# Kernel tuning notes

Hardware: AMD Instinct MI355X
Metric: run time of the kernel (lower is better)

Reference implementation:

```python
import jax, jax.numpy as jnp
import numpy as np

B, CI, CO, H, W = 32, 64, 64, 128, 128
M1, M2 = 32, 32


def setup_inputs() -> dict:
    key = jax.random.key(0)
    kx, k1r, k1i, k2r, k2i = jax.random.split(key, 5)
    scale = 1.0 / (CI * CO)
    x = jax.random.normal(kx, (B, CI, H, W), dtype=jnp.float32)
    mk = lambda k: jax.random.uniform(k, (CI, CO, M1, M2), dtype=jnp.float32,
                                      minval=-scale, maxval=scale)
    return {"x": x, "w1r": mk(k1r), "w1i": mk(k1i), "w2r": mk(k2r), "w2i": mk(k2i)}


def reference(x, w1r, w1i, w2r, w2i):
    # x: [B, CI, H, W] real. Full 2D FFT over the last two dims.
    x_ft = jnp.fft.fft2(x.astype(jnp.complex64))  # [B, CI, H, W]
    w1 = jax.lax.complex(w1r, w1i)  # [CI, CO, M1, M2]
    w2 = jax.lax.complex(w2r, w2i)
    # Truncated-mode complex channel mixing with conjugated weights.
    top = jnp.einsum('bixy,ioxy->boxy', x_ft[:, :, :M1, :M2], jnp.conj(w1))
    bot = jnp.einsum('bixy,ioxy->boxy', x_ft[:, :, -M1:, :M2], jnp.conj(w2))
    # Scatter into rfft-width spectral tensor (as in the original code).
    Wout = W // 2 + 1
    out_ft = jnp.zeros((B, CO, H, Wout), dtype=jnp.complex64)
    out_ft = out_ft.at[:, :, :M1, :M2].set(top)
    out_ft = out_ft.at[:, :, -M1:, :M2].set(bot)
    # Full inverse 2D FFT, take real part. Output: [B, CO, H, Wout].
    return jnp.real(jnp.fft.ifft2(out_ft))
```

## Files before the change

### kernel.cpp

```cpp
#include <hip/hip_runtime.h>
#include <math.h>

#define PI2 6.28318530717958647692f


typedef short bf16x8 __attribute__((ext_vector_type(8)));
typedef float f32x4 __attribute__((ext_vector_type(4)));

static __device__ __forceinline__ ushort f2bf(float f) {
    uint u = __float_as_uint(f);
    u += 0x7FFFu + ((u >> 16) & 1u);
    return (ushort)(u >> 16);
}
static __device__ __forceinline__ float bf2f(ushort h) {
    return __uint_as_float(((uint)h) << 16);
}

__global__ void k_einit(ushort* __restrict__ e1, ushort* __restrict__ e2,
                        ushort* __restrict__ ec, ushort* __restrict__ ew) {
    int id = blockIdx.x * 256 + threadIdx.x;
    if (id < 8192) {
        int w = id & 127, col = id >> 7;
        int ky = col & 31, csel = col >> 5;
        int m = (ky * w) & 127;
        float sv, cv;
        sincosf((float)m * (PI2 / 128.0f), &sv, &cv);
        float val = csel ? -sv : cv;
        ushort hi = f2bf(val);
        int ui = col * 128 + (w ^ ((col & 7) << 3));
        e1[ui] = hi;
        e1[8192 + ui] = f2bf(val - bf2f(hi));
    } else if (id < 16384) {
        int id2 = id - 8192;
        int h = id2 & 127, kxi = id2 >> 7;
        int kx = (kxi < 32) ? kxi : (kxi + 64);
        int m = (kx * h) & 127;
        float sv, cv;
        sincosf((float)m * (PI2 / 128.0f), &sv, &cv);
        float er = cv, ei = -sv;
        int ui = kxi * 128 + (h ^ ((kxi & 7) << 3));
        ushort eh = f2bf(er);
        e2[ui] = eh;
        e2[8192 + ui] = f2bf(er - bf2f(eh));
        ushort ih = f2bf(ei);
        e2[16384 + ui] = ih;
        e2[24576 + ui] = f2bf(ei - bf2f(ih));
    } else if (id < 32768) {
        int id2 = id - 16384;
        int j = id2 & 7, ln = (id2 >> 3) & 15, kq = (id2 >> 7) & 3,
            kk = (id2 >> 9) & 3, mt = id2 >> 11;
        int h = mt * 16 + ln;
        int k = kk * 32 + kq * 8 + j;
        int kc = (k < 64) ? k : (k - 64);
        int kx = (kc < 32) ? kc : (kc + 64);
        int m = (kx * h) & 127;
        float sv, cv;
        sincosf((float)m * (PI2 / 128.0f), &sv, &cv);
        float val = ((k < 64) ? cv : sv) * (1.0f / 8320.0f);
        ushort hi = f2bf(val);
        ec[id2] = hi;
        ec[16384 + id2] = f2bf(val - bf2f(hi));
    } else if (id < 40448) {
        int id3 = id - 32768;
        int off = id3 % 2560, pe = id3 / 2560;
        int j = off & 7, ln = (off >> 3) & 15, kq = (off >> 7) & 3, nt1 = off >> 9;
        int ky = kq * 8 + j, w = nt1 * 16 + ln;
        float val = 0.0f;
        if (w < 65) {
            int m = (w * ky) % 65;
            float sv, cv;
            sincosf((float)m * (PI2 / 65.0f), &sv, &cv);
            val = (pe == 0) ? cv : ((pe == 1) ? sv : -sv);
        }
        ushort hi = f2bf(val);
        ew[pe * 5120 + off] = hi;
        ew[pe * 5120 + 2560 + off] = f2bf(val - bf2f(hi));
    }
}

__global__ __launch_bounds__(256) void k_f1(const float* __restrict__ x,
                                            const ushort* __restrict__ eimg,
                                            ushort* __restrict__ yimg) {
    __shared__ ushort lds[32768];
    const int bi = blockIdx.x;
    const int hbase = blockIdx.y * 64;
    const int t = threadIdx.x;

    {
        const uint4* esrc = (const uint4*)eimg;
        uint4* edst = (uint4*)lds;
        for (int i = t; i < 2048; i += 256) edst[i] = esrc[i];
    }

    const float* xp = x + (size_t)bi * 16384 + (size_t)hbase * 128;
    for (int i = 0; i < 4; i++) {
        int idx = i * 2048 + t * 8;
        int row = idx >> 7, w0 = idx & 127;
        float4 v0 = *(const float4*)&xp[idx];
        float4 v1 = *(const float4*)&xp[idx + 4];
        float vv[8] = {v0.x, v0.y, v0.z, v0.w, v1.x, v1.y, v1.z, v1.w};
        ushort h[8], l[8];
#pragma unroll
        for (int j = 0; j < 8; j++) {
            h[j] = f2bf(vv[j]);
            l[j] = f2bf(vv[j] - bf2f(h[j]));
        }
        uint4 hp, lp;
        hp.x = (uint)h[0] | ((uint)h[1] << 16);
        hp.y = (uint)h[2] | ((uint)h[3] << 16);
        hp.z = (uint)h[4] | ((uint)h[5] << 16);
        hp.w = (uint)h[6] | ((uint)h[7] << 16);
        lp.x = (uint)l[0] | ((uint)l[1] << 16);
        lp.y = (uint)l[2] | ((uint)l[3] << 16);
        lp.z = (uint)l[4] | ((uint)l[5] << 16);
        lp.w = (uint)l[6] | ((uint)l[7] << 16);
        int ui = row * 128 + (w0 ^ ((row & 7) << 3));
        *(uint4*)&lds[16384 + ui] = hp;
        *(uint4*)&lds[24576 + ui] = lp;
    }
    __syncthreads();

    const int lane = t & 63, wid = t >> 6;
    const int ln = lane & 15, kq = lane >> 4;
    f32x4 acc[4] = {};
#pragma unroll
    for (int kk = 0; kk < 4; kk++) {
        int k0 = kk * 32 + kq * 8;
        int arow = wid * 16 + ln;
        int aui = arow * 128 + (k0 ^ ((arow & 7) << 3));
        bf16x8 ah = *(bf16x8*)&lds[16384 + aui];
        bf16x8 al = *(bf16x8*)&lds[24576 + aui];
#pragma unroll
        for (int nt = 0; nt < 4; nt++) {
            int col = nt * 16 + ln;
            int bui = col * 128 + (k0 ^ ((col & 7) << 3));
            bf16x8 bh = *(bf16x8*)&lds[bui];
            bf16x8 bl = *(bf16x8*)&lds[8192 + bui];
            acc[nt] = __builtin_amdgcn_mfma_f32_16x16x32_bf16(ah, bh, acc[nt], 0, 0, 0);
            acc[nt] = __builtin_amdgcn_mfma_f32_16x16x32_bf16(ah, bl, acc[nt], 0, 0, 0);
            acc[nt] = __builtin_amdgcn_mfma_f32_16x16x32_bf16(al, bh, acc[nt], 0, 0, 0);
        }
    }

    ushort* yp = yimg + (size_t)bi * 16384;
    const int h0 = hbase + wid * 16 + kq * 4;
#pragma unroll
    for (int nt = 0; nt < 4; nt++) {
        int col = nt * 16 + ln;
        int ky = col & 31, c = col >> 5;
        ushort4 h4, l4;
        float v0 = acc[nt][0], v1 = acc[nt][1], v2 = acc[nt][2], v3 = acc[nt][3];
        h4.x = f2bf(v0); l4.x = f2bf(v0 - bf2f(h4.x));
        h4.y = f2bf(v1); l4.y = f2bf(v1 - bf2f(h4.y));
        h4.z = f2bf(v2); l4.z = f2bf(v2 - bf2f(h4.z));
        h4.w = f2bf(v3); l4.w = f2bf(v3 - bf2f(h4.w));
        int hs = h0 ^ ((ky & 7) << 3);
        *(ushort4*)&yp[(c * 2) * 4096 + ky * 128 + hs] = h4;
        *(ushort4*)&yp[(c * 2 + 1) * 4096 + ky * 128 + hs] = l4;
    }
}

__global__ __launch_bounds__(512) void k_f2(const ushort* __restrict__ yimg,
                                            const ushort* __restrict__ e2img,
                                            float2* __restrict__ xf) {
    __shared__ ushort lds[32768];
    const int t = threadIdx.x;
    const int bi0 = blockIdx.x * 8;

    uint4 R[4];
    {
        const uint4* ys = (const uint4*)(yimg + (size_t)bi0 * 16384);
#pragma unroll
        for (int c = 0; c < 4; c++) R[c] = ys[c * 512 + t];
    }
    {
        const uint4* es = (const uint4*)e2img;
        uint4* ed = (uint4*)lds;
        for (int i = t; i < 4096; i += 512) ed[i] = es[i];
    }
    __syncthreads();
    const int lane = t & 63, wid = t >> 6;
    const int ln = lane & 15, kq = lane >> 4;
    const int mt = wid >> 1, nt = wid & 1;
    const int arow = mt * 16 + ln;
    const int bcol = nt * 16 + ln;
    bf16x8 Erh[4], Erl[4], Eih[4], Eil[4];
#pragma unroll
    for (int kk = 0; kk < 4; kk++) {
        int k0 = kk * 32 + kq * 8;
        int ao = arow * 128 + (k0 ^ ((arow & 7) << 3));
        Erh[kk] = *(const bf16x8*)&lds[ao];
        Erl[kk] = *(const bf16x8*)&lds[8192 + ao];
        Eih[kk] = *(const bf16x8*)&lds[16384 + ao];
        Eil[kk] = *(const bf16x8*)&lds[24576 + ao];
    }
    __syncthreads();
    {
        uint4* yd = (uint4*)lds;
#pragma unroll
        for (int c = 0; c < 4; c++) yd[c * 512 + t] = R[c];
    }
    __syncthreads();

    int cur = 0;
    for (int j = 0; j < 8; j++) {
        const int bi = bi0 + j;
        if (j < 7) {
            const uint4* ys = (const uint4*)(yimg + (size_t)(bi + 1) * 16384);
#pragma unroll
            for (int c = 0; c < 4; c++) R[c] = ys[c * 512 + t];
        }
        const ushort* yb = &lds[cur * 16384];
        f32x4 P1 = {}, P2 = {}, P3 = {}, P4 = {};
#pragma unroll
        for (int kk = 0; kk < 4; kk++) {
            int k0 = kk * 32 + kq * 8;
            int bo = bcol * 128 + (k0 ^ ((bcol & 7) << 3));
            bf16x8 Yrh = *(const bf16x8*)&yb[bo];
            bf16x8 Yrl = *(const bf16x8*)&yb[4096 + bo];
            bf16x8 Yih = *(const bf16x8*)&yb[8192 + bo];
            bf16x8 Yil = *(const bf16x8*)&yb[12288 + bo];
            P1 = __builtin_amdgcn_mfma_f32_16x16x32_bf16(Erh[kk], Yrh, P1, 0, 0, 0);
            P1 = __builtin_amdgcn_mfma_f32_16x16x32_bf16(Erh[kk], Yrl, P1, 0, 0, 0);
            P1 = __builtin_amdgcn_mfma_f32_16x16x32_bf16(Erl[kk], Yrh, P1, 0, 0, 0);
            P2 = __builtin_amdgcn_mfma_f32_16x16x32_bf16(Eih[kk], Yih, P2, 0, 0, 0);
            P2 = __builtin_amdgcn_mfma_f32_16x16x32_bf16(Eih[kk], Yil, P2, 0, 0, 0);
            P2 = __builtin_amdgcn_mfma_f32_16x16x32_bf16(Eil[kk], Yih, P2, 0, 0, 0);
            P3 = __builtin_amdgcn_mfma_f32_16x16x32_bf16(Erh[kk], Yih, P3, 0, 0, 0);
            P3 = __builtin_amdgcn_mfma_f32_16x16x32_bf16(Erh[kk], Yil, P3, 0, 0, 0);
            P3 = __builtin_amdgcn_mfma_f32_16x16x32_bf16(Erl[kk], Yih, P3, 0, 0, 0);
            P4 = __builtin_amdgcn_mfma_f32_16x16x32_bf16(Eih[kk], Yrh, P4, 0, 0, 0);
            P4 = __builtin_amdgcn_mfma_f32_16x16x32_bf16(Eih[kk], Yrl, P4, 0, 0, 0);
            P4 = __builtin_amdgcn_mfma_f32_16x16x32_bf16(Eil[kk], Yrh, P4, 0, 0, 0);
        }
        float2* xp = xf + (size_t)bi * 2048 + (size_t)(mt * 16 + kq * 4) * 32 + bcol;
#pragma unroll
        for (int r = 0; r < 4; r++)
            xp[(size_t)r * 32] = make_float2(P1[r] - P2[r], P3[r] + P4[r]);
        if (j < 7) {
            uint4* yd = (uint4*)&lds[(cur ^ 1) * 16384];
#pragma unroll
            for (int c = 0; c < 4; c++) yd[c * 512 + t] = R[c];
            __syncthreads();
            cur ^= 1;
        }
    }
}

__global__ __launch_bounds__(512) void k_mix(const float2* __restrict__ xf,
                                             const float* __restrict__ w1r, const float* __restrict__ w1i,
                                             const float* __restrict__ w2r, const float* __restrict__ w2i,
                                             float2* __restrict__ tt) {
    __shared__ float2 xfs[8192];
    const int kxi = blockIdx.x;
    const int b0 = blockIdx.y * 8;
    const int t = threadIdx.x;
    const int ky = t & 31, grp = t >> 5;
    const int o0 = grp * 4;
    const float* wr = (kxi < 32) ? w1r : w2r;
    const float* wi = (kxi < 32) ? w1i : w2i;
    const int kxim = kxi & 31;
    float accr[8][4], acci[8][4];
    for (int jb = 0; jb < 8; jb++)
        for (int jo = 0; jo < 4; jo++) { accr[jb][jo] = 0.0f; acci[jb][jo] = 0.0f; }

    for (int stage = 0; stage < 2; stage++) {
        const int ibase = stage * 32;
        __syncthreads();
        for (int idx = t; idx < 8192; idx += 512) {
            int b = idx >> 10, ii = (idx >> 5) & 31, kk = idx & 31;
            size_t g = ((size_t)(b0 + b) * 64 + (ibase + ii)) * 2048 + (size_t)kxi * 32 + kk;
            xfs[idx] = xf[g];
        }
        __syncthreads();
        for (int ii = 0; ii < 32; ii++) {
            const int i = ibase + ii;
            float wr4[4], wi4[4];
#pragma unroll
            for (int jo = 0; jo < 4; jo++) {
                size_t g = ((size_t)i * 64 + (o0 + jo)) * 1024 + (size_t)kxim * 32 + ky;
                wr4[jo] = wr[g]; wi4[jo] = wi[g];
            }
#pragma unroll
            for (int jb = 0; jb < 8; jb++) {
                float2 xv = xfs[(jb << 10) + (ii << 5) + ky];
#pragma unroll
                for (int jo = 0; jo < 4; jo++) {
                    accr[jb][jo] += xv.x * wr4[jo] + xv.y * wi4[jo];
                    acci[jb][jo] += xv.y * wr4[jo] - xv.x * wi4[jo];
                }
            }
        }
    }
    for (int jb = 0; jb < 8; jb++)
        for (int jo = 0; jo < 4; jo++) {
            size_t g = ((size_t)(b0 + jb) * 64 + (o0 + jo)) * 2048 + (size_t)kxi * 32 + ky;
            tt[g] = make_float2(accr[jb][jo], acci[jb][jo]);
        }
}

#define G1_TILE(TT, ZRv, ZIv)                                                  \
    do {                                                                       \
        int mt1_ = (TT) & 3, nt1_ = (TT) >> 2;                                 \
        int arow_ = mt1_ * 16 + ln;                                            \
        int aad_ = arow_ * 40 + ((kq ^ (arow_ & 3)) << 3);                     \
        bf16x8 TRh_ = *(const bf16x8*)&lds[aad_];                              \
        bf16x8 TRl_ = *(const bf16x8*)&lds[2560 + aad_];                       \
        bf16x8 TIh_ = *(const bf16x8*)&lds[5120 + aad_];                       \
        bf16x8 TIl_ = *(const bf16x8*)&lds[7680 + aad_];                       \
        const ushort* bp_ = ew + (((nt1_ * 4 + kq) * 16 + ln) * 8);            \
        bf16x8 CWh_ = *(const bf16x8*)(bp_);                                   \
        bf16x8 CWl_ = *(const bf16x8*)(bp_ + 2560);                            \
        bf16x8 SWh_ = *(const bf16x8*)(bp_ + 5120);                            \
        bf16x8 SWl_ = *(const bf16x8*)(bp_ + 7680);                            \
        bf16x8 SNh_ = *(const bf16x8*)(bp_ + 10240);                           \
        bf16x8 SNl_ = *(const bf16x8*)(bp_ + 12800);                           \
        ZRv = __builtin_amdgcn_mfma_f32_16x16x32_bf16(TRh_, CWh_, ZRv, 0, 0, 0); \
        ZRv = __builtin_amdgcn_mfma_f32_16x16x32_bf16(TRh_, CWl_, ZRv, 0, 0, 0); \
        ZRv = __builtin_amdgcn_mfma_f32_16x16x32_bf16(TRl_, CWh_, ZRv, 0, 0, 0); \
        ZRv = __builtin_amdgcn_mfma_f32_16x16x32_bf16(TIh_, SNh_, ZRv, 0, 0, 0); \
        ZRv = __builtin_amdgcn_mfma_f32_16x16x32_bf16(TIh_, SNl_, ZRv, 0, 0, 0); \
        ZRv = __builtin_amdgcn_mfma_f32_16x16x32_bf16(TIl_, SNh_, ZRv, 0, 0, 0); \
        ZIv = __builtin_amdgcn_mfma_f32_16x16x32_bf16(TRh_, SWh_, ZIv, 0, 0, 0); \
        ZIv = __builtin_amdgcn_mfma_f32_16x16x32_bf16(TRh_, SWl_, ZIv, 0, 0, 0); \
        ZIv = __builtin_amdgcn_mfma_f32_16x16x32_bf16(TRl_, SWh_, ZIv, 0, 0, 0); \
        ZIv = __builtin_amdgcn_mfma_f32_16x16x32_bf16(TIh_, CWh_, ZIv, 0, 0, 0); \
        ZIv = __builtin_amdgcn_mfma_f32_16x16x32_bf16(TIh_, CWl_, ZIv, 0, 0, 0); \
        ZIv = __builtin_amdgcn_mfma_f32_16x16x32_bf16(TIl_, CWh_, ZIv, 0, 0, 0); \
    } while (0)

#define Z_STORE(TT, ZRv, ZIv)                                                  \
    do {                                                                       \
        int mt1_ = (TT) & 3, nt1_ = (TT) >> 2;                                 \
        int w_ = nt1_ * 16 + ln;                                               \
        int kxi_ = mt1_ * 16 + kq * 4;                                         \
        int octr_ = kxi_ >> 3, sub_ = kxi_ & 7;                                \
        int adr_ = w_ * 128 + ((octr_ ^ (w_ & 7)) << 3) + sub_;                \
        int adi_ = w_ * 128 + (((octr_ + 8) ^ (w_ & 7)) << 3) + sub_;          \
        ushort4 rh_, rl_, ih_, il_;                                            \
        float v0_ = ZRv[0], v1_ = ZRv[1], v2_ = ZRv[2], v3_ = ZRv[3];          \
        rh_.x = f2bf(v0_); rl_.x = f2bf(v0_ - bf2f(rh_.x));                    \
        rh_.y = f2bf(v1_); rl_.y = f2bf(v1_ - bf2f(rh_.y));                    \
        rh_.z = f2bf(v2_); rl_.z = f2bf(v2_ - bf2f(rh_.z));                    \
        rh_.w = f2bf(v3_); rl_.w = f2bf(v3_ - bf2f(rh_.w));                    \
        v0_ = -ZIv[0]; v1_ = -ZIv[1]; v2_ = -ZIv[2]; v3_ = -ZIv[3];            \
        ih_.x = f2bf(v0_); il_.x = f2bf(v0_ - bf2f(ih_.x));                    \
        ih_.y = f2bf(v1_); il_.y = f2bf(v1_ - bf2f(ih_.y));                    \
        ih_.z = f2bf(v2_); il_.z = f2bf(v2_ - bf2f(ih_.z));                    \
        ih_.w = f2bf(v3_); il_.w = f2bf(v3_ - bf2f(ih_.w));                    \
        *(ushort4*)&lds[adr_] = rh_;                                           \
        *(ushort4*)&lds[10240 + adr_] = rl_;                                   \
        *(ushort4*)&lds[adi_] = ih_;                                           \
        *(ushort4*)&lds[10240 + adi_] = il_;                                   \
    } while (0)

__global__ __launch_bounds__(512) void k_inv(const float2* __restrict__ tt,
                                             const ushort* __restrict__ ec,
                                             const ushort* __restrict__ ew,
                                             float* __restrict__ out) {
    __shared__ ushort lds[20480];
    const int bo = blockIdx.x, t = threadIdx.x;
    const int lane = t & 63, wid = t >> 6;
    const int ln = lane & 15, kq = lane >> 4;

    bf16x8 ECh[4], ECl[4];
#pragma unroll
    for (int kk = 0; kk < 4; kk++) {
        const ushort* p = ec + ((((wid * 4 + kk) * 4 + kq) * 16 + ln) * 8);
        ECh[kk] = *(const bf16x8*)p;
        ECl[kk] = *(const bf16x8*)(p + 16384);
    }

    const float2* tp = tt + (size_t)bo * 2048;
    for (int i = t; i < 2048; i += 512) {
        float2 v = tp[i];
        int row = i >> 5, ky = i & 31;
        int ad = row * 40 + ((((ky >> 3) ^ (row & 3))) << 3) + (ky & 7);
        ushort rh = f2bf(v.x), ih = f2bf(v.y);
        lds[ad] = rh;
        lds[2560 + ad] = f2bf(v.x - bf2f(rh));
        lds[5120 + ad] = ih;
        lds[7680 + ad] = f2bf(v.y - bf2f(ih));
    }
    __syncthreads();

    f32x4 ZR0 = {}, ZI0 = {}, ZR1 = {}, ZI1 = {}, ZR2 = {}, ZI2 = {};
    G1_TILE(wid, ZR0, ZI0);
    G1_TILE(wid + 8, ZR1, ZI1);
    if (wid < 4) G1_TILE(wid + 16, ZR2, ZI2);
    __syncthreads();

    Z_STORE(wid, ZR0, ZI0);
    Z_STORE(wid + 8, ZR1, ZI1);
    if (wid < 4) Z_STORE(wid + 16, ZR2, ZI2);
    __syncthreads();

    f32x4 acc[5] = {};
#pragma unroll
    for (int nt = 0; nt < 5; nt++) {
        int w = nt * 16 + ln;
#pragma unroll
        for (int kk = 0; kk < 4; kk++) {
            int oct = kk * 4 + kq;
            int ad = w * 128 + ((oct ^ (w & 7)) << 3);
            bf16x8 Bh = *(const bf16x8*)&lds[ad];
            bf16x8 Bl = *(const bf16x8*)&lds[10240 + ad];
            acc[nt] = __builtin_amdgcn_mfma_f32_16x16x32_bf16(ECh[kk], Bh, acc[nt], 0, 0, 0);
            acc[nt] = __builtin_amdgcn_mfma_f32_16x16x32_bf16(ECh[kk], Bl, acc[nt], 0, 0, 0);
            acc[nt] = __builtin_amdgcn_mfma_f32_16x16x32_bf16(ECl[kk], Bh, acc[nt], 0, 0, 0);
        }
    }
    float* op = out + (size_t)bo * 8320;
    const int h0 = wid * 16 + kq * 4;
#pragma unroll
    for (int nt = 0; nt < 5; nt++) {
        int w = nt * 16 + ln;
        if (w < 65) {
#pragma unroll
            for (int r = 0; r < 4; r++)
                op[(h0 + r) * 65 + w] = acc[nt][r];
        }
    }
}

extern "C" void kernel_launch(void* const* d_in, const int* in_sizes, int n_in,
                              void* d_out, int out_size, void* d_ws, size_t ws_size,
                              hipStream_t stream) {
    const float* x   = (const float*)d_in[0];
    const float* w1r = (const float*)d_in[1];
    const float* w1i = (const float*)d_in[2];
    const float* w2r = (const float*)d_in[3];
    const float* w2i = (const float*)d_in[4];
    float2* ws = (float2*)d_ws;

    ushort* yimg = (ushort*)ws;
    float2* ta   = ws;
    float2* xfa  = ws + 8388608;
    ushort* e1img = (ushort*)(ws + 12582912);
    ushort* e2img = (ushort*)(ws + 12587008);
    ushort* ecimg = (ushort*)(ws + 12595200);
    ushort* ewimg = (ushort*)(ws + 12603392);
    float* out = (float*)d_out;

    k_einit<<<160, 256, 0, stream>>>(e1img, e2img, ecimg, ewimg);
    k_f1<<<dim3(2048, 2), 256, 0, stream>>>(x, e1img, yimg);
    k_f2<<<256, 512, 0, stream>>>(yimg, e2img, xfa);
    k_mix<<<dim3(64, 4), 512, 0, stream>>>(xfa, w1r, w1i, w2r, w2i, ta);
    k_inv<<<2048, 512, 0, stream>>>(ta, ecimg, ewimg, out);
}
```

Before: 401.2 us.

## Rewrite spectral channel mixing as split-bf16 MFMA GEMMs with mode-major layout

```diff
diff --git a/kernel.cpp b/kernel.cpp
--- a/kernel.cpp
+++ b/kernel.cpp
@@ -233,10 +233,10 @@
             P4 = __builtin_amdgcn_mfma_f32_16x16x32_bf16(Eih[kk], Yrl, P4, 0, 0, 0);
             P4 = __builtin_amdgcn_mfma_f32_16x16x32_bf16(Eil[kk], Yrh, P4, 0, 0, 0);
         }
-        float2* xp = xf + (size_t)bi * 2048 + (size_t)(mt * 16 + kq * 4) * 32 + bcol;
+        float2* xp = xf + (size_t)(mt * 16 + kq * 4) * 65536 + (size_t)bi * 32 + bcol;
 #pragma unroll
         for (int r = 0; r < 4; r++)
-            xp[(size_t)r * 32] = make_float2(P1[r] - P2[r], P3[r] + P4[r]);
+            xp[(size_t)r * 65536] = make_float2(P1[r] - P2[r], P3[r] + P4[r]);
         if (j < 7) {
             uint4* yd = (uint4*)&lds[(cur ^ 1) * 16384];
 #pragma unroll
@@ -247,56 +247,93 @@
     }
 }
 
-__global__ __launch_bounds__(512) void k_mix(const float2* __restrict__ xf,
+__global__ __launch_bounds__(256) void k_mix(const float2* __restrict__ xf,
                                              const float* __restrict__ w1r, const float* __restrict__ w1i,
                                              const float* __restrict__ w2r, const float* __restrict__ w2i,
                                              float2* __restrict__ tt) {
-    __shared__ float2 xfs[8192];
+    __shared__ ushort lds[24576];
     const int kxi = blockIdx.x;
-    const int b0 = blockIdx.y * 8;
+    const int ky  = blockIdx.y;
     const int t = threadIdx.x;
-    const int ky = t & 31, grp = t >> 5;
-    const int o0 = grp * 4;
     const float* wr = (kxi < 32) ? w1r : w2r;
     const float* wi = (kxi < 32) ? w1i : w2i;
     const int kxim = kxi & 31;
-    float accr[8][4], acci[8][4];
-    for (int jb = 0; jb < 8; jb++)
-        for (int jo = 0; jo < 4; jo++) { accr[jb][jo] = 0.0f; acci[jb][jo] = 0.0f; }
-
-    for (int stage = 0; stage < 2; stage++) {
-        const int ibase = stage * 32;
-        __syncthreads();
-        for (int idx = t; idx < 8192; idx += 512) {
-            int b = idx >> 10, ii = (idx >> 5) & 31, kk = idx & 31;
-            size_t g = ((size_t)(b0 + b) * 64 + (ibase + ii)) * 2048 + (size_t)kxi * 32 + kk;
-            xfs[idx] = xf[g];
-        }
-        __syncthreads();
-        for (int ii = 0; ii < 32; ii++) {
-            const int i = ibase + ii;
-            float wr4[4], wi4[4];
-#pragma unroll
-            for (int jo = 0; jo < 4; jo++) {
-                size_t g = ((size_t)i * 64 + (o0 + jo)) * 1024 + (size_t)kxim * 32 + ky;
-                wr4[jo] = wr[g]; wi4[jo] = wi[g];
-            }
-#pragma unroll
-            for (int jb = 0; jb < 8; jb++) {
-                float2 xv = xfs[(jb << 10) + (ii << 5) + ky];
-#pragma unroll
-                for (int jo = 0; jo < 4; jo++) {
-                    accr[jb][jo] += xv.x * wr4[jo] + xv.y * wi4[jo];
-                    acci[jb][jo] += xv.y * wr4[jo] - xv.x * wi4[jo];
-                }
-            }
-        }
-    }
-    for (int jb = 0; jb < 8; jb++)
-        for (int jo = 0; jo < 4; jo++) {
-            size_t g = ((size_t)(b0 + jb) * 64 + (o0 + jo)) * 2048 + (size_t)kxi * 32 + ky;
-            tt[g] = make_float2(accr[jb][jo], acci[jb][jo]);
-        }
+
+    const float2* xp = xf + (size_t)kxi * 65536 + ky;
+#pragma unroll
+    for (int k = 0; k < 8; k++) {
+        int idx = t + 256 * k;
+        float2 v = xp[(size_t)idx * 32];
+        int b = idx >> 6, i = idx & 63;
+        int ad = b * 64 + ((((i >> 3) ^ (b & 7))) << 3) + (i & 7);
+        ushort rh = f2bf(v.x), ih = f2bf(v.y);
+        lds[ad] = rh;
+        lds[2048 + ad] = f2bf(v.x - bf2f(rh));
+        lds[4096 + ad] = ih;
+        lds[6144 + ad] = f2bf(v.y - bf2f(ih));
+    }
+    const size_t wbase = (size_t)kxim * 32 + ky;
+#pragma unroll
+    for (int k = 0; k < 16; k++) {
+        int p = t + 256 * k;
+        int o = p >> 6, i = p & 63;
+        size_t g = ((size_t)i * 64 + o) * 1024 + wbase;
+        float wrv = wr[g], wiv = wi[g];
+        int ad = 8192 + o * 64 + ((((i >> 3) ^ (o & 7))) << 3) + (i & 7);
+        ushort rh = f2bf(wrv), ih = f2bf(wiv);
+        lds[ad] = rh;
+        lds[4096 + ad] = f2bf(wrv - bf2f(rh));
+        lds[8192 + ad] = ih;
+        lds[12288 + ad] = f2bf(wiv - bf2f(ih));
+    }
+    __syncthreads();
+
+    const int lane = t & 63, wid = t >> 6;
+    const int ln = lane & 15, kq = lane >> 4;
+    const int mt = wid & 1;
+    f32x4 Tr[2] = {}, TiA[2] = {}, TiB[2] = {};
+#pragma unroll
+    for (int u = 0; u < 2; u++) {
+        int nt = (wid >> 1) + u * 2;
+        int o = nt * 16 + ln;
+        int b = mt * 16 + ln;
+#pragma unroll
+        for (int kk = 0; kk < 2; kk++) {
+            int aad = b * 64 + (((kk * 4 + kq) ^ (b & 7)) << 3);
+            bf16x8 Xrh = *(const bf16x8*)&lds[aad];
+            bf16x8 Xrl = *(const bf16x8*)&lds[2048 + aad];
+            bf16x8 Xih = *(const bf16x8*)&lds[4096 + aad];
+            bf16x8 Xil = *(const bf16x8*)&lds[6144 + aad];
+            int bad = 8192 + o * 64 + (((kk * 4 + kq) ^ (o & 7)) << 3);
+            bf16x8 Wrh = *(const bf16x8*)&lds[bad];
+            bf16x8 Wrl = *(const bf16x8*)&lds[4096 + bad];
+            bf16x8 Wih = *(const bf16x8*)&lds[8192 + bad];
+            bf16x8 Wil = *(const bf16x8*)&lds[12288 + bad];
+            Tr[u] = __builtin_amdgcn_mfma_f32_16x16x32_bf16(Xrh, Wrh, Tr[u], 0, 0, 0);
+            Tr[u] = __builtin_amdgcn_mfma_f32_16x16x32_bf16(Xrh, Wrl, Tr[u], 0, 0, 0);
+            Tr[u] = __builtin_amdgcn_mfma_f32_16x16x32_bf16(Xrl, Wrh, Tr[u], 0, 0, 0);
+            Tr[u] = __builtin_amdgcn_mfma_f32_16x16x32_bf16(Xih, Wih, Tr[u], 0, 0, 0);
+            Tr[u] = __builtin_amdgcn_mfma_f32_16x16x32_bf16(Xih, Wil, Tr[u], 0, 0, 0);
+            Tr[u] = __builtin_amdgcn_mfma_f32_16x16x32_bf16(Xil, Wih, Tr[u], 0, 0, 0);
+            TiA[u] = __builtin_amdgcn_mfma_f32_16x16x32_bf16(Xih, Wrh, TiA[u], 0, 0, 0);
+            TiA[u] = __builtin_amdgcn_mfma_f32_16x16x32_bf16(Xih, Wrl, TiA[u], 0, 0, 0);
+            TiA[u] = __builtin_amdgcn_mfma_f32_16x16x32_bf16(Xil, Wrh, TiA[u], 0, 0, 0);
+            TiB[u] = __builtin_amdgcn_mfma_f32_16x16x32_bf16(Xrh, Wih, TiB[u], 0, 0, 0);
+            TiB[u] = __builtin_amdgcn_mfma_f32_16x16x32_bf16(Xrh, Wil, TiB[u], 0, 0, 0);
+            TiB[u] = __builtin_amdgcn_mfma_f32_16x16x32_bf16(Xrl, Wih, TiB[u], 0, 0, 0);
+        }
+    }
+    float2* top = tt + ((size_t)kxi * 32 + ky) * 2048;
+#pragma unroll
+    for (int u = 0; u < 2; u++) {
+        int nt = (wid >> 1) + u * 2;
+        int o = nt * 16 + ln;
+#pragma unroll
+        for (int r = 0; r < 4; r++) {
+            int b = mt * 16 + kq * 4 + r;
+            top[b * 64 + o] = make_float2(Tr[u][r], TiA[u][r] - TiB[u][r]);
+        }
+    }
 }
 
 #define G1_TILE(TT, ZRv, ZIv)                                                  \
@@ -371,9 +408,9 @@
         ECl[kk] = *(const bf16x8*)(p + 16384);
     }
 
-    const float2* tp = tt + (size_t)bo * 2048;
+    const float2* tp = tt + bo;
     for (int i = t; i < 2048; i += 512) {
-        float2 v = tp[i];
+        float2 v = tp[(size_t)i * 2048];
         int row = i >> 5, ky = i & 31;
         int ad = row * 40 + ((((ky >> 3) ^ (row & 3))) << 3) + (ky & 7);
         ushort rh = f2bf(v.x), ih = f2bf(v.y);
@@ -445,6 +482,6 @@
     k_einit<<<160, 256, 0, stream>>>(e1img, e2img, ecimg, ewimg);
     k_f1<<<dim3(2048, 2), 256, 0, stream>>>(x, e1img, yimg);
     k_f2<<<256, 512, 0, stream>>>(yimg, e2img, xfa);
-    k_mix<<<dim3(64, 4), 512, 0, stream>>>(xfa, w1r, w1i, w2r, w2i, ta);
+    k_mix<<<dim3(64, 32), 256, 0, stream>>>(xfa, w1r, w1i, w2r, w2i, ta);
     k_inv<<<2048, 512, 0, stream>>>(ta, ecimg, ewimg, out);
 }
```

Measured after the change: 475.6 us. +18.5%, slower.
